# Kernel optimization log

Measured on AMD Instinct MI355X. Metric: run time of the kernel, lower is better.

Reference implementation:

```python
import jax, jax.numpy as jnp
import numpy as np

MUL0, MUL1 = 64, 32      # multiplicities of 0e scalars and 1o vectors
N = 200000               # number of nodes
EPS = 1e-8
LOG2 = float(np.log(2.0))


def setup_inputs() -> dict:
    key = jax.random.key(0)
    ks = jax.random.split(key, 9)
    f32 = jnp.float32
    return {
        "node_input": jax.random.normal(ks[0], (N, MUL0 + 3 * MUL1), f32),  # 64x0e + 32x1o
        "node_attr": jax.random.normal(ks[1], (N, 1), f32),                  # 1x0e
        "field": jax.random.normal(ks[2], (N, 3), f32),                      # 1x1o
        "W_tp_0e": jax.random.normal(ks[3], (MUL1, MUL0), f32),  # path 1o(x)1o->0e
        "W_tp_1o": jax.random.normal(ks[4], (MUL0, MUL1), f32),  # path 0e(x)1o->1o
        "W_lin_0e": jax.random.normal(ks[5], (MUL0, MUL0), f32),
        "W_lin_1o": jax.random.normal(ks[6], (MUL1, MUL1), f32),
        "W_sc_0e": jax.random.normal(ks[7], (MUL0, MUL0), f32),
        "W_sc_1o": jax.random.normal(ks[8], (MUL1, MUL1), f32),
    }


def _ssp(x):
    # shift_softplus
    return jax.nn.softplus(x) - LOG2


def reference(node_input, node_attr, field, W_tp_0e, W_tp_1o, W_lin_0e, W_lin_1o, W_sc_0e, W_sc_1o):
    x0 = node_input[:, :MUL0]                        # [N,64]  0e scalars
    x1 = node_input[:, MUL0:].reshape(-1, MUL1, 3)   # [N,32,3] 1o vectors

    # tp = FullyConnectedTensorProduct(input, 1x1o -> output)
    # e3nn 'component' irrep norm + 'element' path norm:
    # path 1o(x)1o->0e : w3j = I/sqrt(3), alpha = 1/mul1  -> coef 1/sqrt(3*mul1)
    t0 = (1.0 / np.sqrt(3.0 * MUL1)) * jnp.einsum('num,nm,uw->nw', x1, field, W_tp_0e)   # [N,64]
    # path 0e(x)1o->1o : w3j = I/sqrt(3), alpha = 3/mul0 -> coef 1/sqrt(mul0)
    t1 = (1.0 / np.sqrt(MUL0)) * jnp.einsum('nu,nm,uw->nwm', x0, field, W_tp_1o)         # [N,32,3]

    # lin2 = Linear(tp.irreps_out.simplify() -> output): per-irrep block linear, coef 1/sqrt(fan_in)
    y0 = (1.0 / np.sqrt(MUL0)) * (t0 @ W_lin_0e)                                          # [N,64]
    y1 = (1.0 / np.sqrt(MUL1)) * jnp.einsum('num,uw->nwm', t1, W_lin_1o)                  # [N,32,3]

    # sc = FCTP(features, 1x0e attr -> output): scalar-gated per-irrep linear, coef 1/sqrt(mul)
    a = node_attr[:, 0]
    z0 = (1.0 / np.sqrt(MUL0)) * jnp.einsum('nu,n,uw->nw', y0, a, W_sc_0e)
    z1 = (1.0 / np.sqrt(MUL1)) * jnp.einsum('num,n,uw->nwm', y1, a, W_sc_1o)

    # residual
    r0 = x0 + z0
    r1 = x1 + z1

    # NormActivation(shift_softplus, normalize=True, epsilon=1e-8, bias=False)
    n0 = jnp.sqrt(r0 * r0 + EPS * EPS)                          # [N,64]
    o0 = r0 * (_ssp(n0) / n0)
    n1 = jnp.sqrt(jnp.sum(r1 * r1, axis=-1) + EPS * EPS)        # [N,32]
    o1 = r1 * (_ssp(n1) / n1)[..., None]

    return jnp.concatenate([o0, o1.reshape(-1, 3 * MUL1)], axis=-1)   # [N,160]
```

## Files before the change

kernel.cpp:

```cpp
#include <hip/hip_runtime.h>
#include <math.h>

#define MUL0 64
#define MUL1 32
#define ROW_F 160
#define EPS2 1.0e-16f
#define LOG2F_ 0.69314718055994531f
#define LP 65
#define WPB 2
#define TPB (WPB * 64)

#define OT0   0
#define OL0   2048
#define OS0   6144
#define OT1   10240
#define OL1   12288
#define OS1   13312
#define OM0   14336
#define OM1   16384
#define CW_LDS 18432

__global__ __launch_bounds__(1024)
void combine_weights(const float* __restrict__ Wtp0,
                     const float* __restrict__ Wtp1,
                     const float* __restrict__ Wlin0,
                     const float* __restrict__ Wlin1,
                     const float* __restrict__ Wsc0,
                     const float* __restrict__ Wsc1,
                     float* __restrict__ ws)
{
    __shared__ float L[CW_LDS];
    const int t = threadIdx.x;

    {
        const float* srcs[6] = {Wtp0, Wlin0, Wsc0, Wtp1, Wlin1, Wsc1};
        const int    offs[6] = {OT0, OL0, OS0, OT1, OL1, OS1};
        const int    n4s[6]  = {512, 1024, 1024, 512, 256, 256};
#pragma unroll
        for (int m = 0; m < 6; ++m) {
            const float4* s = (const float4*)srcs[m];
            float4* d = (float4*)(L + offs[m]);
            for (int i = t; i < n4s[m]; i += 1024) d[i] = s[i];
        }
    }
    __syncthreads();

    if (t < 512) {
        const int u = t >> 4, q = t & 15;
        float4 acc = {0.f, 0.f, 0.f, 0.f};
#pragma unroll 8
        for (int k = 0; k < 64; ++k) {
            const float a = L[OT0 + u * 64 + k];
            const float4 b = ((const float4*)(L + OL0))[k * 16 + q];
            acc.x += a * b.x; acc.y += a * b.y; acc.z += a * b.z; acc.w += a * b.w;
        }
        ((float4*)(L + OM0))[u * 16 + q] = acc;
    } else {
        const int t2 = t - 512;
        const int u = t2 >> 3, q = t2 & 7;
        float4 acc = {0.f, 0.f, 0.f, 0.f};
#pragma unroll 8
        for (int k = 0; k < 32; ++k) {
            const float a = L[OT1 + u * 32 + k];
            const float4 b = ((const float4*)(L + OL1))[k * 8 + q];
            acc.x += a * b.x; acc.y += a * b.y; acc.z += a * b.z; acc.w += a * b.w;
        }
        ((float4*)(L + OM1))[u * 8 + q] = acc;
    }
    __syncthreads();

    const float C0 = 1.0f / (sqrtf(96.0f) * 64.0f);
    const float C1 = 1.0f / 256.0f;
    if (t < 512) {
        const int u = t >> 4, q = t & 15;
        float4 acc = {0.f, 0.f, 0.f, 0.f};
#pragma unroll 8
        for (int k = 0; k < 64; ++k) {
            const float a = L[OM0 + u * 64 + k];
            const float4 b = ((const float4*)(L + OS0))[k * 16 + q];
            acc.x += a * b.x; acc.y += a * b.y; acc.z += a * b.z; acc.w += a * b.w;
        }
        acc.x *= C0; acc.y *= C0; acc.z *= C0; acc.w *= C0;
        ((float4*)ws)[u * 16 + q] = acc;
    } else {
        const int t2 = t - 512;
        const int u = t2 >> 3, q = t2 & 7;
        float4 acc = {0.f, 0.f, 0.f, 0.f};
#pragma unroll 8
        for (int k = 0; k < 32; ++k) {
            const float a = L[OM1 + u * 32 + k];
            const float4 b = ((const float4*)(L + OS1))[k * 8 + q];
            acc.x += a * b.x; acc.y += a * b.y; acc.z += a * b.z; acc.w += a * b.w;
        }
        acc.x *= C1; acc.y *= C1; acc.z *= C1; acc.w *= C1;
        ((float4*)(ws + 2048))[u * 8 + q] = acc;
    }
}

__device__ __forceinline__ float ssp_over_n(float n)
{
    float sp = n + __logf(1.0f + __expf(-n)) - LOG2F_;
    return __fdividef(sp, n);
}

__device__ __forceinline__ void wave_fence()
{
    __asm__ volatile("" ::: "memory");
    __builtin_amdgcn_wave_barrier();
}

template<int W>
struct Stage {
    float4 v[W / 4];

    __device__ __forceinline__ void issue(const float* __restrict__ g,
                                          int lane, int rmax)
    {
        constexpr int NF4 = W / 4;
#pragma unroll
        for (int k = 0; k < NF4; ++k) {
            int id = k * 64 + lane;
            int r = id / NF4, gg = id % NF4;
            int rr = r <= rmax ? r : rmax;
            v[k] = *(const float4*)(g + rr * ROW_F + 4 * gg);
        }
    }

    __device__ __forceinline__ void commitL(float* buf, int lane)
    {
        constexpr int NF4 = W / 4;
        wave_fence();
#pragma unroll
        for (int k = 0; k < NF4; ++k) {
            int id = k * 64 + lane;
            int r = id / NF4, gg = id % NF4;
            buf[(4 * gg + 0) * LP + r] = v[k].x;
            buf[(4 * gg + 1) * LP + r] = v[k].y;
            buf[(4 * gg + 2) * LP + r] = v[k].z;
            buf[(4 * gg + 3) * LP + r] = v[k].w;
        }
        wave_fence();
    }
};

template<int W>
__device__ __forceinline__ void flushL(float* __restrict__ g, const float* buf,
                                       int lane, int rmax)
{
    constexpr int NF4 = W / 4;
    wave_fence();
#pragma unroll
    for (int k = 0; k < NF4; ++k) {
        int id = k * 64 + lane;
        int r = id / NF4, gg = id % NF4;
        int rr = r <= rmax ? r : rmax;
        float4 o;
        o.x = buf[(4 * gg + 0) * LP + r];
        o.y = buf[(4 * gg + 1) * LP + r];
        o.z = buf[(4 * gg + 2) * LP + r];
        o.w = buf[(4 * gg + 3) * LP + r];
        *(float4*)(g + rr * ROW_F + 4 * gg) = o;
    }
}

__global__ __launch_bounds__(TPB) __attribute__((amdgpu_waves_per_eu(3, 3)))
void field_main(const float* __restrict__ in,
                const float* __restrict__ attr,
                const float* __restrict__ field,
                const float* __restrict__ Wg,
                float* __restrict__ out,
                int nrows)
{
    __shared__ float tbuf[WPB][48 * LP];

    const int tid = threadIdx.x;
    const int wv = tid >> 6, lane = tid & 63;
    int r0 = (blockIdx.x * WPB + wv) * 64;
    if (r0 > nrows - 64) r0 = nrows - 64;
    if (r0 < 0) r0 = 0;
    const int rmax = min(63, nrows - 1 - r0);
    const int rowe = r0 + min(lane, rmax);

    const float a  = attr[rowe];
    const float f0 = field[3 * rowe + 0];
    const float f1 = field[3 * rowe + 1];
    const float f2 = field[3 * rowe + 2];
    const float af0 = a * f0, af1 = a * f1, af2 = a * f2;

    const float* gin  = in  + (size_t)r0 * ROW_F;
    float*       gout = out + (size_t)r0 * ROW_F;
    float* buf = tbuf[wv];

    Stage<32> XA, XB;
    Stage<48> C0;
    XA.issue(gin,      lane, rmax);
    XB.issue(gin + 32, lane, rmax);
    C0.issue(gin + 64, lane, rmax);

    float pw[32];
#pragma unroll
    for (int w = 0; w < 32; ++w) pw[w] = 0.f;

    XA.commitL(buf, lane);
#pragma unroll 2
    for (int u = 0; u < 32; ++u) {
        const float xu = buf[u * LP + lane];
        const float4* wr = (const float4*)(Wg + 2048 + u * 32);
#pragma unroll
        for (int j = 0; j < 8; ++j) {
            const float4 t = wr[j];
            pw[4 * j + 0] += xu * t.x;
            pw[4 * j + 1] += xu * t.y;
            pw[4 * j + 2] += xu * t.z;
            pw[4 * j + 3] += xu * t.w;
        }
    }
    XB.commitL(buf, lane);
#pragma unroll 2
    for (int u = 0; u < 32; ++u) {
        const float xu = buf[u * LP + lane];
        const float4* wr = (const float4*)(Wg + 3072 + u * 32);
#pragma unroll
        for (int j = 0; j < 8; ++j) {
            const float4 t = wr[j];
            pw[4 * j + 0] += xu * t.x;
            pw[4 * j + 1] += xu * t.y;
            pw[4 * j + 2] += xu * t.z;
            pw[4 * j + 3] += xu * t.w;
        }
    }
#pragma unroll
    for (int w = 0; w < 32; ++w) pw[w] *= a;

    float s1[32];
    Stage<48> C1;

    C0.commitL(buf, lane);
    C1.issue(gin + 64 + 48, lane, rmax);
#pragma unroll
    for (int i = 0; i < 16; ++i) {
        const float m0 = buf[(3 * i + 0) * LP + lane];
        const float m1 = buf[(3 * i + 1) * LP + lane];
        const float m2 = buf[(3 * i + 2) * LP + lane];
        s1[i] = m0 * af0 + m1 * af1 + m2 * af2;
        const float p = pw[i];
        float q0 = m0 + p * f0;
        float q1 = m1 + p * f1;
        float q2 = m2 + p * f2;
        float n = sqrtf(q0 * q0 + q1 * q1 + q2 * q2 + EPS2);
        float t = ssp_over_n(n);
        buf[(3 * i + 0) * LP + lane] = q0 * t;
        buf[(3 * i + 1) * LP + lane] = q1 * t;
        buf[(3 * i + 2) * LP + lane] = q2 * t;
    }
    flushL<48>(gout + 64, buf, lane, rmax);

    C1.commitL(buf, lane);
#pragma unroll
    for (int i = 0; i < 16; ++i) {
        const float m0 = buf[(3 * i + 0) * LP + lane];
        const float m1 = buf[(3 * i + 1) * LP + lane];
        const float m2 = buf[(3 * i + 2) * LP + lane];
        s1[16 + i] = m0 * af0 + m1 * af1 + m2 * af2;
        const float p = pw[16 + i];
        float q0 = m0 + p * f0;
        float q1 = m1 + p * f1;
        float q2 = m2 + p * f2;
        float n = sqrtf(q0 * q0 + q1 * q1 + q2 * q2 + EPS2);
        float t = ssp_over_n(n);
        buf[(3 * i + 0) * LP + lane] = q0 * t;
        buf[(3 * i + 1) * LP + lane] = q1 * t;
        buf[(3 * i + 2) * LP + lane] = q2 * t;
    }
    flushL<48>(gout + 64 + 48, buf, lane, rmax);

    wave_fence();
#pragma unroll
    for (int i = 0; i < 32; ++i) buf[i * LP + lane] = s1[i];
    wave_fence();

    Stage<32> XR0, XR1;
    XR0.issue(gin,      lane, rmax);
    XR1.issue(gin + 32, lane, rmax);

    float acc0[32], acc1[32];
#pragma unroll
    for (int j = 0; j < 32; ++j) { acc0[j] = 0.f; acc1[j] = 0.f; }
#pragma unroll 2
    for (int u = 0; u < 32; ++u) {
        const float su = buf[u * LP + lane];
        const float4* wr = (const float4*)(Wg + u * 64);
#pragma unroll
        for (int j = 0; j < 8; ++j) {
            const float4 t = wr[j];
            acc0[4 * j + 0] += su * t.x;
            acc0[4 * j + 1] += su * t.y;
            acc0[4 * j + 2] += su * t.z;
            acc0[4 * j + 3] += su * t.w;
        }
#pragma unroll
        for (int j = 0; j < 8; ++j) {
            const float4 t = wr[8 + j];
            acc1[4 * j + 0] += su * t.x;
            acc1[4 * j + 1] += su * t.y;
            acc1[4 * j + 2] += su * t.z;
            acc1[4 * j + 3] += su * t.w;
        }
    }

    XR0.commitL(buf, lane);
#pragma unroll
    for (int j = 0; j < 32; ++j) {
        const float r = buf[j * LP + lane] + acc0[j];
        const float n = sqrtf(r * r + EPS2);
        buf[j * LP + lane] = r * ssp_over_n(n);
    }
    flushL<32>(gout, buf, lane, rmax);

    XR1.commitL(buf, lane);
#pragma unroll
    for (int j = 0; j < 32; ++j) {
        const float r = buf[j * LP + lane] + acc1[j];
        const float n = sqrtf(r * r + EPS2);
        buf[j * LP + lane] = r * ssp_over_n(n);
    }
    flushL<32>(gout + 32, buf, lane, rmax);
}

extern "C" void kernel_launch(void* const* d_in, const int* in_sizes, int n_in,
                              void* d_out, int out_size, void* d_ws, size_t ws_size,
                              hipStream_t stream)
{
    const float* node_input = (const float*)d_in[0];
    const float* node_attr  = (const float*)d_in[1];
    const float* field      = (const float*)d_in[2];
    const float* Wtp0       = (const float*)d_in[3];
    const float* Wtp1       = (const float*)d_in[4];
    const float* Wlin0      = (const float*)d_in[5];
    const float* Wlin1      = (const float*)d_in[6];
    const float* Wsc0       = (const float*)d_in[7];
    const float* Wsc1       = (const float*)d_in[8];
    float* out = (float*)d_out;
    float* ws  = (float*)d_ws;

    const int nrows = in_sizes[0] / ROW_F;

    hipLaunchKernelGGL(combine_weights, dim3(1), dim3(1024), 0, stream,
                       Wtp0, Wtp1, Wlin0, Wlin1, Wsc0, Wsc1, ws);

    const int nwaves = (nrows + 63) / 64;
    const int nb = (nwaves + WPB - 1) / WPB;
    hipLaunchKernelGGL(field_main, dim3(nb), dim3(TPB), 0, stream,
                       node_input, node_attr, field, ws, out, nrows);
}
```

Measured before the change: 350.8 us.

## Restructure vector stage into smaller chunks and split final matmul to cut registers

Splits the 1o vector processing into four 24-column chunks with a double-buffered prefetch, in place of two 48-column stages. The final scalar matmul now uses one 32-wide accumulator computed twice, once per output half, instead of two live accumulators. Half the s1 values stay in registers and half go through LDS. The fixed waves-per-EU attribute is removed, so the compiler can choose occupancy from the lower register pressure. The trade-off is that the first half of s1 is read twice from registers and more, smaller loads are issued.

```diff
diff --git a/kernel.cpp b/kernel.cpp
--- a/kernel.cpp
+++ b/kernel.cpp
@@ -163,7 +163,7 @@
     }
 }
 
-__global__ __launch_bounds__(TPB) __attribute__((amdgpu_waves_per_eu(3, 3)))
+__global__ __launch_bounds__(TPB)
 void field_main(const float* __restrict__ in,
                 const float* __restrict__ attr,
                 const float* __restrict__ field,
@@ -192,16 +192,18 @@
     float* buf = tbuf[wv];
 
     Stage<32> XA, XB;
-    Stage<48> C0;
     XA.issue(gin,      lane, rmax);
     XB.issue(gin + 32, lane, rmax);
-    C0.issue(gin + 64, lane, rmax);
+
+    XA.commitL(buf, lane);
+
+    Stage<24> CA, CB;
+    CA.issue(gin + 64, lane, rmax);
 
     float pw[32];
 #pragma unroll
     for (int w = 0; w < 32; ++w) pw[w] = 0.f;
 
-    XA.commitL(buf, lane);
 #pragma unroll 2
     for (int u = 0; u < 32; ++u) {
         const float xu = buf[u * LP + lane];
@@ -233,94 +235,119 @@
     for (int w = 0; w < 32; ++w) pw[w] *= a;
 
     float s1[32];
-    Stage<48> C1;
-
-    C0.commitL(buf, lane);
-    C1.issue(gin + 64 + 48, lane, rmax);
-#pragma unroll
+
+#define X1_CHUNK(CUR, NXT, CIDX, DO_PREFETCH)                                  \
+    {                                                                          \
+        CUR.commitL(buf, lane);                                                \
+        if (DO_PREFETCH) NXT.issue(gin + 64 + 24 * ((CIDX) + 1), lane, rmax);  \
+        _Pragma("unroll")                                                      \
+        for (int i = 0; i < 8; ++i) {                                          \
+            const int u = 8 * (CIDX) + i;                                      \
+            const float m0 = buf[(3 * i + 0) * LP + lane];                     \
+            const float m1 = buf[(3 * i + 1) * LP + lane];                     \
+            const float m2 = buf[(3 * i + 2) * LP + lane];                     \
+            s1[u] = m0 * af0 + m1 * af1 + m2 * af2;                            \
+            const float p = pw[u];                                             \
+            float q0 = m0 + p * f0;                                            \
+            float q1 = m1 + p * f1;                                            \
+            float q2 = m2 + p * f2;                                            \
+            float n = sqrtf(q0 * q0 + q1 * q1 + q2 * q2 + EPS2);               \
+            float t = ssp_over_n(n);                                           \
+            buf[(3 * i + 0) * LP + lane] = q0 * t;                             \
+            buf[(3 * i + 1) * LP + lane] = q1 * t;                             \
+            buf[(3 * i + 2) * LP + lane] = q2 * t;                             \
+        }                                                                      \
+        flushL<24>(gout + 64 + 24 * (CIDX), buf, lane, rmax);                  \
+    }
+
+    X1_CHUNK(CA, CB, 0, true)
+    X1_CHUNK(CB, CA, 1, true)
+    X1_CHUNK(CA, CB, 2, true)
+    X1_CHUNK(CB, CA, 3, false)
+#undef X1_CHUNK
+
+    wave_fence();
+#pragma unroll
+    for (int i = 0; i < 16; ++i) buf[(32 + i) * LP + lane] = s1[16 + i];
+    wave_fence();
+
+    Stage<32> XR;
+    XR.issue(gin, lane, rmax);
+
+    float acc[32];
+#pragma unroll
+    for (int j = 0; j < 32; ++j) acc[j] = 0.f;
+#pragma unroll
+    for (int u = 0; u < 16; ++u) {
+        const float su = s1[u];
+        const float4* wr = (const float4*)(Wg + u * 64);
+#pragma unroll
+        for (int j = 0; j < 8; ++j) {
+            const float4 t = wr[j];
+            acc[4 * j + 0] += su * t.x;
+            acc[4 * j + 1] += su * t.y;
+            acc[4 * j + 2] += su * t.z;
+            acc[4 * j + 3] += su * t.w;
+        }
+    }
+#pragma unroll 2
     for (int i = 0; i < 16; ++i) {
-        const float m0 = buf[(3 * i + 0) * LP + lane];
-        const float m1 = buf[(3 * i + 1) * LP + lane];
-        const float m2 = buf[(3 * i + 2) * LP + lane];
-        s1[i] = m0 * af0 + m1 * af1 + m2 * af2;
-        const float p = pw[i];
-        float q0 = m0 + p * f0;
-        float q1 = m1 + p * f1;
-        float q2 = m2 + p * f2;
-        float n = sqrtf(q0 * q0 + q1 * q1 + q2 * q2 + EPS2);
-        float t = ssp_over_n(n);
-        buf[(3 * i + 0) * LP + lane] = q0 * t;
-        buf[(3 * i + 1) * LP + lane] = q1 * t;
-        buf[(3 * i + 2) * LP + lane] = q2 * t;
-    }
-    flushL<48>(gout + 64, buf, lane, rmax);
-
-    C1.commitL(buf, lane);
-#pragma unroll
-    for (int i = 0; i < 16; ++i) {
-        const float m0 = buf[(3 * i + 0) * LP + lane];
-        const float m1 = buf[(3 * i + 1) * LP + lane];
-        const float m2 = buf[(3 * i + 2) * LP + lane];
-        s1[16 + i] = m0 * af0 + m1 * af1 + m2 * af2;
-        const float p = pw[16 + i];
-        float q0 = m0 + p * f0;
-        float q1 = m1 + p * f1;
-        float q2 = m2 + p * f2;
-        float n = sqrtf(q0 * q0 + q1 * q1 + q2 * q2 + EPS2);
-        float t = ssp_over_n(n);
-        buf[(3 * i + 0) * LP + lane] = q0 * t;
-        buf[(3 * i + 1) * LP + lane] = q1 * t;
-        buf[(3 * i + 2) * LP + lane] = q2 * t;
-    }
-    flushL<48>(gout + 64 + 48, buf, lane, rmax);
-
-    wave_fence();
-#pragma unroll
-    for (int i = 0; i < 32; ++i) buf[i * LP + lane] = s1[i];
-    wave_fence();
-
-    Stage<32> XR0, XR1;
-    XR0.issue(gin,      lane, rmax);
-    XR1.issue(gin + 32, lane, rmax);
-
-    float acc0[32], acc1[32];
-#pragma unroll
-    for (int j = 0; j < 32; ++j) { acc0[j] = 0.f; acc1[j] = 0.f; }
-#pragma unroll 2
-    for (int u = 0; u < 32; ++u) {
-        const float su = buf[u * LP + lane];
-        const float4* wr = (const float4*)(Wg + u * 64);
-#pragma unroll
-        for (int j = 0; j < 8; ++j) {
-            const float4 t = wr[j];
-            acc0[4 * j + 0] += su * t.x;
-            acc0[4 * j + 1] += su * t.y;
-            acc0[4 * j + 2] += su * t.z;
-            acc0[4 * j + 3] += su * t.w;
-        }
-#pragma unroll
-        for (int j = 0; j < 8; ++j) {
-            const float4 t = wr[8 + j];
-            acc1[4 * j + 0] += su * t.x;
-            acc1[4 * j + 1] += su * t.y;
-            acc1[4 * j + 2] += su * t.z;
-            acc1[4 * j + 3] += su * t.w;
-        }
-    }
-
-    XR0.commitL(buf, lane);
+        const float su = buf[(32 + i) * LP + lane];
+        const float4* wr = (const float4*)(Wg + (16 + i) * 64);
+#pragma unroll
+        for (int j = 0; j < 8; ++j) {
+            const float4 t = wr[j];
+            acc[4 * j + 0] += su * t.x;
+            acc[4 * j + 1] += su * t.y;
+            acc[4 * j + 2] += su * t.z;
+            acc[4 * j + 3] += su * t.w;
+        }
+    }
+
+    XR.commitL(buf, lane);
+    Stage<32> XS;
+    XS.issue(gin + 32, lane, rmax);
 #pragma unroll
     for (int j = 0; j < 32; ++j) {
-        const float r = buf[j * LP + lane] + acc0[j];
+        const float r = buf[j * LP + lane] + acc[j];
         const float n = sqrtf(r * r + EPS2);
         buf[j * LP + lane] = r * ssp_over_n(n);
     }
     flushL<32>(gout, buf, lane, rmax);
 
-    XR1.commitL(buf, lane);
+#pragma unroll
+    for (int j = 0; j < 32; ++j) acc[j] = 0.f;
+#pragma unroll
+    for (int u = 0; u < 16; ++u) {
+        const float su = s1[u];
+        const float4* wr = (const float4*)(Wg + u * 64 + 32);
+#pragma unroll
+        for (int j = 0; j < 8; ++j) {
+            const float4 t = wr[j];
+            acc[4 * j + 0] += su * t.x;
+            acc[4 * j + 1] += su * t.y;
+            acc[4 * j + 2] += su * t.z;
+            acc[4 * j + 3] += su * t.w;
+        }
+    }
+#pragma unroll 2
+    for (int i = 0; i < 16; ++i) {
+        const float su = buf[(32 + i) * LP + lane];
+        const float4* wr = (const float4*)(Wg + (16 + i) * 64 + 32);
+#pragma unroll
+        for (int j = 0; j < 8; ++j) {
+            const float4 t = wr[j];
+            acc[4 * j + 0] += su * t.x;
+            acc[4 * j + 1] += su * t.y;
+            acc[4 * j + 2] += su * t.z;
+            acc[4 * j + 3] += su * t.w;
+        }
+    }
+
+    XS.commitL(buf, lane);
 #pragma unroll
     for (int j = 0; j < 32; ++j) {
-        const float r = buf[j * LP + lane] + acc1[j];
+        const float r = buf[j * LP + lane] + acc[j];
         const float n = sqrtf(r * r + EPS2);
         buf[j * LP + lane] = r * ssp_over_n(n);
     }
```

New measurement: 320.8 us. 1.09x faster.
